# Kernel tuning notes

Measured on AMD Instinct MI355X. Metric: run time of the kernel, lower is better.

Reference implementation:

```python
import jax, jax.numpy as jnp
import numpy as np

B, D, K, N = 32, 512, 64, 4096
EPS = 1e-12


def setup_inputs() -> dict:
    key = jax.random.key(0)
    k1, k2, k3, k4 = jax.random.split(key, 4)
    featureVolume = jax.random.normal(k1, (B, D, N), dtype=jnp.float32)
    conv_w = jax.random.normal(k2, (K, D), dtype=jnp.float32) * (1.0 / np.sqrt(D))
    conv_b = jax.random.normal(k3, (K,), dtype=jnp.float32) * 0.01
    centers = jax.random.normal(k4, (D, K), dtype=jnp.float32)
    return {"featureVolume": featureVolume, "conv_w": conv_w, "conv_b": conv_b, "centers": centers}


def reference(featureVolume, conv_w, conv_b, centers):
    # 1x1 conv over length dim -> scores [B, K, N]
    scores = jnp.einsum('kd,bdn->bkn', conv_w, featureVolume) + conv_b[None, :, None]
    soft = jax.nn.softmax(scores, axis=1)                       # softmax over clusters K
    # VLAD aggregation without the B*D*K*N intermediate:
    # sum_n soft[b,k,n] * (x[b,d,n] - c[d,k])
    agg = jnp.einsum('bdn,bkn->bdk', featureVolume, soft)       # [B, D, K]
    agg = agg - centers[None, :, :] * jnp.sum(soft, axis=-1)[:, None, :]
    # intra-normalize over D (torch F.normalize, dim=1)
    norm1 = jnp.linalg.norm(agg, axis=1, keepdims=True)
    agg = agg / jnp.maximum(norm1, EPS)
    # flatten + global L2 normalize
    desc = agg.reshape(agg.shape[0], -1)                        # [B, D*K]
    norm2 = jnp.linalg.norm(desc, axis=1, keepdims=True)
    return desc / jnp.maximum(norm2, EPS)
```

## Files before the change

kernel.cpp:

```cpp
#include <hip/hip_runtime.h>
#include <hip/hip_bf16.h>

#define B_ 32
#define D_ 512
#define K_ 64
#define N_ 4096

typedef __attribute__((ext_vector_type(8))) short short8;
typedef __attribute__((ext_vector_type(4))) short short4v;
typedef __attribute__((ext_vector_type(4))) float f32x4;

static __device__ __forceinline__ unsigned short f2bf(float f) {
    __hip_bfloat16 h = __float2bfloat16(f);
    return *reinterpret_cast<unsigned short*>(&h);
}
static __device__ __forceinline__ float bf2f(unsigned short u) {
    return __uint_as_float(((unsigned)u) << 16);
}

#define SMEM_BYTES 156672
#define WL_OFF 0
#define XL_OFF 65536
#define XT_OFF 131072
#define PT_OFF 147456
#define SXC_OFF 155648

__global__ __launch_bounds__(512, 2) void vlad_fused(const float* __restrict__ X,
                                                     const float* __restrict__ W,
                                                     const float* __restrict__ bias,
                                                     float* __restrict__ aggs,
                                                     float* __restrict__ ssp) {
    extern __shared__ char smem[];
    char* WLp = smem + WL_OFF;
    char* XLp = smem + XL_OFF;
    char* XTp = smem + XT_OFF;
    char* PTp = smem + PT_OFF;
    float2* sxc = (float2*)(smem + SXC_OFF);

    const int ns = blockIdx.x;
    const int b  = blockIdx.y;
    const int t  = threadIdx.x;
    const int w  = t >> 6;
    const int l  = t & 63;
    const int lg = l >> 4;
    const int lr = l & 15;
    const int strip = w & 3;
    const int khalf = w >> 2;

    const int dq2 = t >> 4;
    const int nq  = t & 15;
    const float* Xbase = X + (size_t)b * D_ * N_ + ns * 512 + nq * 4;

    float4 Sa[4], Sb[4];
#pragma unroll
    for (int s = 0; s < 4; ++s) {
        const float* Xs = Xbase + (size_t)(s * 64 + dq2 * 2) * N_;
        Sa[s] = *(const float4*)&Xs[0];
        Sb[s] = *(const float4*)&Xs[N_];
    }

#pragma unroll 4
    for (int j = 0; j < 16; ++j) {
        const int idx = t + j * 512;
        const int k = idx >> 7;
        const int cf = idx & 127;
        const float4 wv = *(const float4*)&W[k * D_ + cf * 4];
        const int C = cf >> 1;
        const int swz = (C & ~7) | ((C ^ k) & 7);
        short4v pk;
        pk[0] = (short)f2bf(wv.x); pk[1] = (short)f2bf(wv.y);
        pk[2] = (short)f2bf(wv.z); pk[3] = (short)f2bf(wv.w);
        *(short4v*)(WLp + k * 1024 + (swz << 4) + (cf & 1) * 8) = pk;
    }

    float bias_r[2][4];
#pragma unroll
    for (int ktl = 0; ktl < 2; ++ktl)
#pragma unroll
        for (int r = 0; r < 4; ++r)
            bias_r[ktl][r] = bias[khalf * 32 + ktl * 16 + lg * 4 + r];

    f32x4 aacc[4][4];
#pragma unroll
    for (int m = 0; m < 4; ++m)
#pragma unroll
        for (int kt = 0; kt < 4; ++kt) {
            aacc[m][kt][0] = 0.f; aacc[m][kt][1] = 0.f;
            aacc[m][kt][2] = 0.f; aacc[m][kt][3] = 0.f;
        }
    float ss_acc = 0.f;

    auto stage_write = [&](int buf, int dglob0, const float4& r0, const float4& r1) {
        const float e0[4] = {r0.x, r0.y, r0.z, r0.w};
        const float e1[4] = {r1.x, r1.y, r1.z, r1.w};
        {
            short4v pk;
            pk[0] = (short)f2bf(e0[0]); pk[1] = (short)f2bf(e0[1]);
            pk[2] = (short)f2bf(e0[2]); pk[3] = (short)f2bf(e0[3]);
            const int d = dglob0;
            *(short4v*)(XLp + d * 128 + ((((nq >> 1) ^ d) & 7) << 4) + (nq & 1) * 8) = pk;
        }
        {
            short4v pk;
            pk[0] = (short)f2bf(e1[0]); pk[1] = (short)f2bf(e1[1]);
            pk[2] = (short)f2bf(e1[2]); pk[3] = (short)f2bf(e1[3]);
            const int d = dglob0 + 1;
            *(short4v*)(XLp + d * 128 + ((((nq >> 1) ^ d) & 7) << 4) + (nq & 1) * 8) = pk;
        }
#pragma unroll
        for (int c = 0; c < 4; ++c) {
            const int n = nq * 4 + c;
            const unsigned v = (unsigned)f2bf(e0[c]) | ((unsigned)f2bf(e1[c]) << 16);
            *(unsigned*)(XTp + buf * 8192 + n * 128 +
                         ((((dq2 >> 2) ^ n) & 7) << 4) + (dq2 & 3) * 4) = v;
        }
    };

    __syncthreads();

    for (int nt = 0; nt < 8; ++nt) {
        f32x4 sacc[2];
#pragma unroll
        for (int ktl = 0; ktl < 2; ++ktl) {
            sacc[ktl][0] = 0.f; sacc[ktl][1] = 0.f; sacc[ktl][2] = 0.f; sacc[ktl][3] = 0.f;
        }

#pragma unroll
        for (int dsl = 0; dsl < 8; ++dsl) {
            const int slot = dsl & 3;
            const int cur  = dsl & 1;
            stage_write(cur, dsl * 64 + dq2 * 2, Sa[slot], Sb[slot]);
            __syncthreads();
            const int s4 = nt * 8 + dsl + 4;
            if (s4 < 64) {
                const int nt2 = s4 >> 3, d2 = s4 & 7;
                const float* Xs = Xbase + nt2 * 64 + (size_t)(d2 * 64 + dq2 * 2) * N_;
                Sa[slot] = *(const float4*)&Xs[0];
                Sb[slot] = *(const float4*)&Xs[N_];
            }
            const int n = strip * 16 + lr;
#pragma unroll
            for (int kc = 0; kc < 2; ++kc) {
                const int bC = kc * 4 + lg;
                const short8 bfrag = *(const short8*)(XTp + cur * 8192 + n * 128 +
                                                      (((bC ^ n) & 7) << 4));
#pragma unroll
                for (int ktl = 0; ktl < 2; ++ktl) {
                    const int k = khalf * 32 + ktl * 16 + lr;
                    const int aC = dsl * 8 + kc * 4 + lg;
                    const int swz = (aC & ~7) | ((aC ^ k) & 7);
                    const short8 afrag = *(const short8*)(WLp + k * 1024 + (swz << 4));
                    sacc[ktl] = __builtin_amdgcn_mfma_f32_16x16x32_bf16(afrag, bfrag, sacc[ktl], 0, 0, 0);
                }
            }
        }

        float p[2][4];
        float cw = -1e30f;
#pragma unroll
        for (int ktl = 0; ktl < 2; ++ktl)
#pragma unroll
            for (int r = 0; r < 4; ++r) {
                p[ktl][r] = sacc[ktl][r] + bias_r[ktl][r];
                cw = fmaxf(cw, p[ktl][r]);
            }
        cw = fmaxf(cw, __shfl_xor(cw, 16));
        cw = fmaxf(cw, __shfl_xor(cw, 32));
        float sum = 0.f;
#pragma unroll
        for (int ktl = 0; ktl < 2; ++ktl)
#pragma unroll
            for (int r = 0; r < 4; ++r) { p[ktl][r] = __expf(p[ktl][r] - cw); sum += p[ktl][r]; }
        sum += __shfl_xor(sum, 16);
        sum += __shfl_xor(sum, 32);
        if (l < 16) sxc[w * 16 + lr] = make_float2(cw, sum);
        __syncthreads();
        const float2 other = sxc[(w ^ 4) * 16 + lr];
        const float cstar = fmaxf(cw, other.x);
        const float e_own = __expf(cw - cstar);
        const float e_oth = __expf(other.x - cstar);
        const float scale = e_own / (sum * e_own + other.y * e_oth);

        {
            const int n = strip * 16 + lr;
#pragma unroll
            for (int ktl = 0; ktl < 2; ++ktl)
#pragma unroll
                for (int r = 0; r < 4; ++r) {
                    const int k = khalf * 32 + ktl * 16 + lg * 4 + r;
                    *(unsigned short*)(PTp + k * 128 + ((((n >> 3) ^ k) & 7) << 4) + (n & 7) * 2) =
                        f2bf(p[ktl][r] * scale);
                }
        }
        __syncthreads();

        {
            const int kk = t >> 3;
            const int c  = t & 7;
            const short8 v = *(const short8*)(PTp + kk * 128 + (((c ^ kk) & 7) << 4));
#pragma unroll
            for (int e = 0; e < 8; ++e) ss_acc += bf2f((unsigned short)v[e]);
        }

#pragma unroll
        for (int kc = 0; kc < 2; ++kc) {
#pragma unroll
            for (int m = 0; m < 4; ++m) {
                const int d = w * 64 + m * 16 + lr;
                const int aC = kc * 4 + lg;
                const short8 afrag = *(const short8*)(XLp + d * 128 + (((aC ^ d) & 7) << 4));
#pragma unroll
                for (int kt = 0; kt < 4; ++kt) {
                    const int k = kt * 16 + lr;
                    const short8 bfrag = *(const short8*)(PTp + k * 128 + (((aC ^ k) & 7) << 4));
                    aacc[m][kt] = __builtin_amdgcn_mfma_f32_16x16x32_bf16(afrag, bfrag, aacc[m][kt], 0, 0, 0);
                }
            }
        }
        __syncthreads();
    }

    float* ag = aggs + ((size_t)ns * B_ + b) * (D_ * K_);
#pragma unroll
    for (int m = 0; m < 4; ++m)
#pragma unroll
        for (int kt = 0; kt < 4; ++kt)
#pragma unroll
            for (int r = 0; r < 4; ++r)
                ag[(size_t)(w * 64 + m * 16 + lg * 4 + r) * K_ + kt * 16 + lr] = aacc[m][kt][r];

    ss_acc += __shfl_xor(ss_acc, 1);
    ss_acc += __shfl_xor(ss_acc, 2);
    ss_acc += __shfl_xor(ss_acc, 4);
    if ((t & 7) == 0) ssp[((size_t)b * 8 + ns) * K_ + (t >> 3)] = ss_acc;
}

__global__ __launch_bounds__(256) void vlad_norm1(const float* __restrict__ aggs,
                                                  const float* __restrict__ centers,
                                                  const float* __restrict__ ssp,
                                                  float* __restrict__ aggsum,
                                                  float* __restrict__ nrmp) {
    const int ds = blockIdx.x;
    const int b  = blockIdx.y;
    const int t  = threadIdx.x;
    const int k  = t & 63;
    const int dg = t >> 6;

    __shared__ float red[4][64];

    float s0 = ssp[((size_t)b * 8 + dg) * K_ + k] + ssp[((size_t)b * 8 + dg + 4) * K_ + k];
    red[dg][k] = s0;
    __syncthreads();
    const float s = red[0][k] + red[1][k] + red[2][k] + red[3][k];
    __syncthreads();

    float sq = 0.f;
    for (int d = ds * 64 + dg; d < ds * 64 + 64; d += 4) {
        float v = -centers[d * K_ + k] * s;
#pragma unroll
        for (int i = 0; i < 8; ++i)
            v += aggs[((size_t)i * B_ + b) * (D_ * K_) + (size_t)d * K_ + k];
        aggsum[((size_t)b * D_ + d) * K_ + k] = v;
        sq = fmaf(v, v, sq);
    }
    red[dg][k] = sq;
    __syncthreads();
    if (t < 64) nrmp[((size_t)b * 8 + ds) * K_ + k] =
        red[0][k] + red[1][k] + red[2][k] + red[3][k];
}

__global__ __launch_bounds__(256) void vlad_norm2(const float* __restrict__ aggsum,
                                                  const float* __restrict__ nrmp,
                                                  float* __restrict__ out) {
    const int ds = blockIdx.x;
    const int b  = blockIdx.y;
    const int t  = threadIdx.x;
    const int k  = t & 63;
    const int dg = t >> 6;

    __shared__ float inv1s[64];
    __shared__ float col2[64];
    __shared__ float inv2s;

    if (t < 64) {
        float tt = 0.f;
#pragma unroll
        for (int i = 0; i < 8; ++i) tt += nrmp[((size_t)b * 8 + i) * K_ + k];
        const float n1 = sqrtf(tt);
        const float i1 = 1.f / fmaxf(n1, 1e-12f);
        inv1s[k] = i1;
        const float c2 = n1 * i1;
        col2[k] = c2 * c2;
    }
    __syncthreads();
    if (t == 0) {
        float tt = 0.f;
        for (int kk = 0; kk < 64; ++kk) tt += col2[kk];
        inv2s = 1.f / fmaxf(sqrtf(tt), 1e-12f);
    }
    __syncthreads();
    const float i12 = inv1s[k] * inv2s;
    for (int d = ds * 64 + dg; d < ds * 64 + 64; d += 4)
        out[(size_t)b * (D_ * K_) + (size_t)d * K_ + k] =
            aggsum[((size_t)b * D_ + d) * K_ + k] * i12;
}

extern "C" void kernel_launch(void* const* d_in, const int* in_sizes, int n_in,
                              void* d_out, int out_size, void* d_ws, size_t ws_size,
                              hipStream_t stream) {
    const float* X       = (const float*)d_in[0];
    const float* W       = (const float*)d_in[1];
    const float* bias    = (const float*)d_in[2];
    const float* centers = (const float*)d_in[3];
    float* out = (float*)d_out;

    char* ws = (char*)d_ws;
    const size_t aggBytes = (size_t)B_ * D_ * K_ * sizeof(float);
    float* aggs   = (float*)ws;
    float* aggsum = (float*)(ws + 8 * aggBytes);
    float* ssp    = (float*)(ws + 9 * aggBytes);
    float* nrmp   = (float*)(ws + 9 * aggBytes + 65536);

    hipFuncSetAttribute((const void*)vlad_fused,
                        hipFuncAttributeMaxDynamicSharedMemorySize, SMEM_BYTES);

    vlad_fused<<<dim3(8, B_), 512, SMEM_BYTES, stream>>>(X, W, bias, aggs, ssp);
    vlad_norm1<<<dim3(8, B_), 256, 0, stream>>>(aggs, centers, ssp, aggsum, nrmp);
    vlad_norm2<<<dim3(8, B_), 256, 0, stream>>>(aggsum, nrmp, out);
}
```

Baseline: 86.41 us.

## Double-buffer X staging with one barrier per slice and register-accumulate softmax sums

Restructures the score-GEMM loop so the next d-slice is converted and written into the alternate LDS buffer while MFMAs run on the current one, leaving one barrier per slice instead of a write-then-sync pattern. It adds an extra XOR term to the transposed-X swizzle to cut LDS bank conflicts, and hoists the P fragments out of the m loop in the aggregation GEMM. The per-cluster soft sums are now accumulated in registers from the values already computed, replacing a separate LDS read pass. This enlarges the ssp partial buffer fourfold and makes norm1 sum more partials, and the extra live registers could reduce occupancy.

```diff
diff --git a/kernel.cpp b/kernel.cpp
--- a/kernel.cpp
+++ b/kernel.cpp
@@ -88,7 +88,11 @@
             aacc[m][kt][0] = 0.f; aacc[m][kt][1] = 0.f;
             aacc[m][kt][2] = 0.f; aacc[m][kt][3] = 0.f;
         }
-    float ss_acc = 0.f;
+    float ssr[2][4];
+#pragma unroll
+    for (int ktl = 0; ktl < 2; ++ktl)
+#pragma unroll
+        for (int r = 0; r < 4; ++r) ssr[ktl][r] = 0.f;
 
     auto stage_write = [&](int buf, int dglob0, const float4& r0, const float4& r1) {
         const float e0[4] = {r0.x, r0.y, r0.z, r0.w};
@@ -107,43 +111,59 @@
             const int d = dglob0 + 1;
             *(short4v*)(XLp + d * 128 + ((((nq >> 1) ^ d) & 7) << 4) + (nq & 1) * 8) = pk;
         }
+        const int C = dq2 >> 2;
 #pragma unroll
         for (int c = 0; c < 4; ++c) {
             const int n = nq * 4 + c;
+            const int sw = (C ^ (n & 7) ^ ((n >> 3) & 7)) & 7;
             const unsigned v = (unsigned)f2bf(e0[c]) | ((unsigned)f2bf(e1[c]) << 16);
-            *(unsigned*)(XTp + buf * 8192 + n * 128 +
-                         ((((dq2 >> 2) ^ n) & 7) << 4) + (dq2 & 3) * 4) = v;
+            *(unsigned*)(XTp + buf * 8192 + n * 128 + (sw << 4) + (dq2 & 3) * 4) = v;
         }
     };
 
     __syncthreads();
 
     for (int nt = 0; nt < 8; ++nt) {
-        f32x4 sacc[2];
-#pragma unroll
-        for (int ktl = 0; ktl < 2; ++ktl) {
-            sacc[ktl][0] = 0.f; sacc[ktl][1] = 0.f; sacc[ktl][2] = 0.f; sacc[ktl][3] = 0.f;
-        }
-
-#pragma unroll
-        for (int dsl = 0; dsl < 8; ++dsl) {
-            const int slot = dsl & 3;
-            const int cur  = dsl & 1;
-            stage_write(cur, dsl * 64 + dq2 * 2, Sa[slot], Sb[slot]);
-            __syncthreads();
-            const int s4 = nt * 8 + dsl + 4;
+        const int base = nt * 8;
+
+        stage_write(0, 0 * 64 + dq2 * 2, Sa[0], Sb[0]);
+        {
+            const int s4 = base + 4;
             if (s4 < 64) {
                 const int nt2 = s4 >> 3, d2 = s4 & 7;
                 const float* Xs = Xbase + nt2 * 64 + (size_t)(d2 * 64 + dq2 * 2) * N_;
-                Sa[slot] = *(const float4*)&Xs[0];
-                Sb[slot] = *(const float4*)&Xs[N_];
+                Sa[0] = *(const float4*)&Xs[0];
+                Sb[0] = *(const float4*)&Xs[N_];
+            }
+        }
+        __syncthreads();
+
+        f32x4 sacc[2];
+#pragma unroll
+        for (int ktl = 0; ktl < 2; ++ktl) {
+            sacc[ktl][0] = 0.f; sacc[ktl][1] = 0.f; sacc[ktl][2] = 0.f; sacc[ktl][3] = 0.f;
+        }
+
+#pragma unroll
+        for (int dsl = 0; dsl < 8; ++dsl) {
+            const int cur = dsl & 1;
+            if (dsl < 7) {
+                const int slot = (dsl + 1) & 3;
+                stage_write(cur ^ 1, (dsl + 1) * 64 + dq2 * 2, Sa[slot], Sb[slot]);
+                const int s5 = base + dsl + 5;
+                if (s5 < 64) {
+                    const int nt2 = s5 >> 3, d2 = s5 & 7;
+                    const float* Xs = Xbase + nt2 * 64 + (size_t)(d2 * 64 + dq2 * 2) * N_;
+                    Sa[slot] = *(const float4*)&Xs[0];
+                    Sb[slot] = *(const float4*)&Xs[N_];
+                }
             }
             const int n = strip * 16 + lr;
 #pragma unroll
             for (int kc = 0; kc < 2; ++kc) {
                 const int bC = kc * 4 + lg;
-                const short8 bfrag = *(const short8*)(XTp + cur * 8192 + n * 128 +
-                                                      (((bC ^ n) & 7) << 4));
+                const int sw = (bC ^ (n & 7) ^ ((n >> 3) & 7)) & 7;
+                const short8 bfrag = *(const short8*)(XTp + cur * 8192 + n * 128 + (sw << 4));
 #pragma unroll
                 for (int ktl = 0; ktl < 2; ++ktl) {
                     const int k = khalf * 32 + ktl * 16 + lr;
@@ -153,6 +173,7 @@
                     sacc[ktl] = __builtin_amdgcn_mfma_f32_16x16x32_bf16(afrag, bfrag, sacc[ktl], 0, 0, 0);
                 }
             }
+            if (dsl < 7) __syncthreads();
         }
 
         float p[2][4];
@@ -188,33 +209,29 @@
 #pragma unroll
                 for (int r = 0; r < 4; ++r) {
                     const int k = khalf * 32 + ktl * 16 + lg * 4 + r;
-                    *(unsigned short*)(PTp + k * 128 + ((((n >> 3) ^ k) & 7) << 4) + (n & 7) * 2) =
-                        f2bf(p[ktl][r] * scale);
+                    const unsigned short us = f2bf(p[ktl][r] * scale);
+                    *(unsigned short*)(PTp + k * 128 + ((((n >> 3) ^ k) & 7) << 4) + (n & 7) * 2) = us;
+                    ssr[ktl][r] += bf2f(us);
                 }
         }
         __syncthreads();
 
-        {
-            const int kk = t >> 3;
-            const int c  = t & 7;
-            const short8 v = *(const short8*)(PTp + kk * 128 + (((c ^ kk) & 7) << 4));
-#pragma unroll
-            for (int e = 0; e < 8; ++e) ss_acc += bf2f((unsigned short)v[e]);
-        }
-
 #pragma unroll
         for (int kc = 0; kc < 2; ++kc) {
+            const int aC = kc * 4 + lg;
+            short8 bfr[4];
+#pragma unroll
+            for (int kt = 0; kt < 4; ++kt) {
+                const int kk2 = kt * 16 + lr;
+                bfr[kt] = *(const short8*)(PTp + kk2 * 128 + (((aC ^ kk2) & 7) << 4));
+            }
 #pragma unroll
             for (int m = 0; m < 4; ++m) {
                 const int d = w * 64 + m * 16 + lr;
-                const int aC = kc * 4 + lg;
                 const short8 afrag = *(const short8*)(XLp + d * 128 + (((aC ^ d) & 7) << 4));
 #pragma unroll
-                for (int kt = 0; kt < 4; ++kt) {
-                    const int k = kt * 16 + lr;
-                    const short8 bfrag = *(const short8*)(PTp + k * 128 + (((aC ^ k) & 7) << 4));
-                    aacc[m][kt] = __builtin_amdgcn_mfma_f32_16x16x32_bf16(afrag, bfrag, aacc[m][kt], 0, 0, 0);
-                }
+                for (int kt = 0; kt < 4; ++kt)
+                    aacc[m][kt] = __builtin_amdgcn_mfma_f32_16x16x32_bf16(afrag, bfr[kt], aacc[m][kt], 0, 0, 0);
             }
         }
         __syncthreads();
@@ -229,10 +246,26 @@
             for (int r = 0; r < 4; ++r)
                 ag[(size_t)(w * 64 + m * 16 + lg * 4 + r) * K_ + kt * 16 + lr] = aacc[m][kt][r];
 
-    ss_acc += __shfl_xor(ss_acc, 1);
-    ss_acc += __shfl_xor(ss_acc, 2);
-    ss_acc += __shfl_xor(ss_acc, 4);
-    if ((t & 7) == 0) ssp[((size_t)b * 8 + ns) * K_ + (t >> 3)] = ss_acc;
+#pragma unroll
+    for (int ktl = 0; ktl < 2; ++ktl)
+#pragma unroll
+        for (int r = 0; r < 4; ++r) {
+            float v = ssr[ktl][r];
+            v += __shfl_xor(v, 1);
+            v += __shfl_xor(v, 2);
+            v += __shfl_xor(v, 4);
+            v += __shfl_xor(v, 8);
+            ssr[ktl][r] = v;
+        }
+    if (lr == 0) {
+#pragma unroll
+        for (int ktl = 0; ktl < 2; ++ktl)
+#pragma unroll
+            for (int r = 0; r < 4; ++r) {
+                const int k = khalf * 32 + ktl * 16 + lg * 4 + r;
+                ssp[(((size_t)b * 8 + ns) * 4 + strip) * K_ + k] = ssr[ktl][r];
+            }
+    }
 }
 
 __global__ __launch_bounds__(256) void vlad_norm1(const float* __restrict__ aggs,
@@ -248,7 +281,10 @@
 
     __shared__ float red[4][64];
 
-    float s0 = ssp[((size_t)b * 8 + dg) * K_ + k] + ssp[((size_t)b * 8 + dg + 4) * K_ + k];
+    float s0 = 0.f;
+#pragma unroll
+    for (int j = 0; j < 8; ++j)
+        s0 += ssp[((size_t)b * 32 + dg * 8 + j) * K_ + k];
     red[dg][k] = s0;
     __syncthreads();
     const float s = red[0][k] + red[1][k] + red[2][k] + red[3][k];
@@ -319,7 +355,7 @@
     float* aggs   = (float*)ws;
     float* aggsum = (float*)(ws + 8 * aggBytes);
     float* ssp    = (float*)(ws + 9 * aggBytes);
-    float* nrmp   = (float*)(ws + 9 * aggBytes + 65536);
+    float* nrmp   = (float*)(ws + 9 * aggBytes + 262144);
 
     hipFuncSetAttribute((const void*)vlad_fused,
                         hipFuncAttributeMaxDynamicSharedMemorySize, SMEM_BYTES);
```

Result: faster. 83.80 us (-3.0%).
